# Kernel tuning notes

Measured on AMD Instinct MI355X. Metric: run time of the kernel, lower is better.

Reference implementation:

```python
import jax, jax.numpy as jnp
import numpy as np

B, N, C, H, K = 4, 16384, 256, 8, 64
D = C // H
EPS = 1e-8

def setup_inputs() -> dict:
    key = jax.random.key(0)
    ks = jax.random.split(key, 6)
    scale = 0.02
    return {
        "voxel_features": jax.random.normal(ks[0], (B, N, C), dtype=jnp.float32),
        "cluster_assignments": jax.random.uniform(ks[1], (B, N, K), dtype=jnp.float32),
        "w_qkv": jax.random.normal(ks[2], (C, 3 * C), dtype=jnp.float32) * scale,
        "w_proj": jax.random.normal(ks[3], (C, C), dtype=jnp.float32) * scale,
        "b_proj": jnp.zeros((C,), dtype=jnp.float32),
        "cluster_bias": jax.random.normal(ks[4], (K, K), dtype=jnp.float32) * scale,
    }

def reference(voxel_features, cluster_assignments, w_qkv, w_proj, b_proj, cluster_bias):
    b, n, c = voxel_features.shape
    h, d = H, c // H
    A = cluster_assignments                                  # (B,N,K)
    qkv = (voxel_features @ w_qkv).reshape(b, n, 3, h, d)    # (B,N,3,H,D)
    q = jnp.moveaxis(qkv[:, :, 0], 1, 2)                     # (B,H,N,D)
    k = jnp.moveaxis(qkv[:, :, 1], 1, 2)
    v = jnp.moveaxis(qkv[:, :, 2], 1, 2)
    # cluster mass per (batch, cluster)
    denom = A.sum(axis=1) + EPS                              # (B,K)
    # cluster-pooled K/V: contraction over N (the huge broadcast-sum in torch)
    k_cluster = jnp.einsum('bnk,bhnd->bhkd', A, k) / denom[:, None, :, None]
    v_cluster = jnp.einsum('bnk,bhnd->bhkd', A, v) / denom[:, None, :, None]
    attn = jnp.einsum('bhnd,bhkd->bhnk', q, k_cluster) * (d ** -0.5)
    bias = jnp.einsum('bnk,kl->bnl', A, cluster_bias)        # (B,N,K)
    attn = jax.nn.softmax(attn + bias[:, None, :, :], axis=-1)
    x = jnp.einsum('bhnk,bhkd->bhnd', attn, v_cluster)       # (B,H,N,D)
    x = jnp.moveaxis(x, 1, 2).reshape(b, n, c)               # (B,N,C)
    return x @ w_proj + b_proj
```

## Files before the change

### kernel.cpp

```cpp
#include <hip/hip_runtime.h>

#define NTOK 16384
#define BATCH 4

typedef __attribute__((ext_vector_type(8))) short bf16x8;
typedef __attribute__((ext_vector_type(8))) unsigned short ushort8;
typedef __attribute__((ext_vector_type(4))) float f32x4;

__device__ __forceinline__ unsigned short f2bf(float f) {
  union { float f; unsigned int u; } c; c.f = f;
  unsigned int r = c.u + 0x7fff + ((c.u >> 16) & 1);
  return (unsigned short)(r >> 16);
}

__global__ __launch_bounds__(256) void zero_f(float* __restrict__ p, int n) {
  int i = blockIdx.x * 256 + threadIdx.x;
  if (i < n) p[i] = 0.f;
}

__global__ __launch_bounds__(256) void convx(const float* __restrict__ in,
                                             unsigned short* __restrict__ out,
                                             int n8) {
  for (int i = blockIdx.x * 256 + threadIdx.x; i < n8; i += gridDim.x * 256) {
    float4 a = *(const float4*)(in + 8 * (size_t)i);
    float4 b = *(const float4*)(in + 8 * (size_t)i + 4);
    ushort8 o;
    o[0] = f2bf(a.x); o[1] = f2bf(a.y); o[2] = f2bf(a.z); o[3] = f2bf(a.w);
    o[4] = f2bf(b.x); o[5] = f2bf(b.y); o[6] = f2bf(b.z); o[7] = f2bf(b.w);
    *(ushort8*)(out + 8 * (size_t)i) = o;
  }
}

__global__ __launch_bounds__(256) void convw(const float* __restrict__ w_qkv,
                                             const float* __restrict__ w_proj,
                                             const float* __restrict__ cb,
                                             unsigned short* __restrict__ wqT,
                                             unsigned short* __restrict__ wpT,
                                             unsigned short* __restrict__ cbbT) {
  int n = blockIdx.x, k = threadIdx.x;
  if (n < 768) wqT[n * 256 + k] = f2bf(w_qkv[(size_t)k * 768 + n]);
  else if (n < 1024) wpT[(n - 768) * 256 + k] = f2bf(w_proj[(size_t)k * 256 + (n - 768)]);
  else if (k < 64) {
    for (int j = 0; j < 64; ++j) cbbT[k * 64 + j] = f2bf(cb[j * 64 + k]);
  }
}

template <int ADD_BIAS, int C_BF16>
__global__ __launch_bounds__(256, 2) void gemm_mfma(const unsigned short* __restrict__ Ab,
                                                    const unsigned short* __restrict__ BT,
                                                    const float* __restrict__ bias,
                                                    void* __restrict__ Cv,
                                                    int N, int K, int lda) {
  __shared__ unsigned short As[2][128][72];
  __shared__ unsigned short Bs[2][128][72];
  const int tid = threadIdx.x;
  int flat = blockIdx.y * gridDim.x + blockIdx.x;
  int xc = flat & 7, t = flat >> 3;
  int gx = gridDim.x, ypx = gridDim.y >> 3;
  int bx = t % gx, by = xc * ypx + t / gx;
  const int bn = bx * 128, bm = by * 128;
  const int lane = tid & 63;
  const int wv = tid >> 6;
  const int wm = wv & 1, wn = wv >> 1;
  const int m16 = lane & 15, quad = lane >> 4;

  const int srow = tid >> 1;
  const int scol = (tid & 1) * 32;

  ushort8 ra[4][4], rb[4][4];
  {
    const unsigned short* ga = Ab + (size_t)(bm + srow) * lda + scol;
    const unsigned short* gb = BT + (size_t)(bn + srow) * K + scol;
#pragma unroll
    for (int kt = 0; kt < 4; ++kt)
#pragma unroll
      for (int i = 0; i < 4; ++i) {
        ra[kt][i] = *(const ushort8*)(ga + kt * 64 + 8 * i);
        rb[kt][i] = *(const ushort8*)(gb + kt * 64 + 8 * i);
      }
  }

  f32x4 acc[4][4];
#pragma unroll
  for (int r = 0; r < 4; ++r)
#pragma unroll
    for (int c = 0; c < 4; ++c) acc[r][c] = (f32x4){0.f, 0.f, 0.f, 0.f};

#pragma unroll
  for (int kt = 0; kt < 4; ++kt) {
    const int bufi = kt & 1;
#pragma unroll
    for (int i = 0; i < 4; ++i) {
      *(ushort8*)&As[bufi][srow][scol + 8 * i] = ra[kt][i];
      *(ushort8*)&Bs[bufi][srow][scol + 8 * i] = rb[kt][i];
    }
    __syncthreads();
#pragma unroll
    for (int ks = 0; ks < 64; ks += 32) {
      bf16x8 af[4], bf[4];
#pragma unroll
      for (int r = 0; r < 4; ++r)
        af[r] = *(const bf16x8*)&As[bufi][wm * 64 + r * 16 + m16][ks + quad * 8];
#pragma unroll
      for (int c = 0; c < 4; ++c)
        bf[c] = *(const bf16x8*)&Bs[bufi][wn * 64 + c * 16 + m16][ks + quad * 8];
#pragma unroll
      for (int r = 0; r < 4; ++r)
#pragma unroll
        for (int c = 0; c < 4; ++c)
          acc[r][c] = __builtin_amdgcn_mfma_f32_16x16x32_bf16(af[r], bf[c], acc[r][c], 0, 0, 0);
    }
  }

#pragma unroll
  for (int c = 0; c < 4; ++c) {
    int col = bn + wn * 64 + c * 16 + m16;
    float bv = ADD_BIAS ? bias[col] : 0.f;
#pragma unroll
    for (int r = 0; r < 4; ++r) {
      int row0 = bm + wm * 64 + r * 16 + quad * 4;
#pragma unroll
      for (int i = 0; i < 4; ++i) {
        if (C_BF16)
          ((unsigned short*)Cv)[(size_t)(row0 + i) * N + col] = f2bf(acc[r][c][i] + bv);
        else
          ((float*)Cv)[(size_t)(row0 + i) * N + col] = acc[r][c][i] + bv;
      }
    }
  }
}

__global__ __launch_bounds__(256) void pool_mfma(const float* __restrict__ A,
                                                 const unsigned short* __restrict__ qkv,
                                                 float* __restrict__ part) {
  __shared__ unsigned short At[64][40];
  __shared__ unsigned short KVt[128][40];
  const int tid = threadIdx.x;
  const int tch = blockIdx.x, cblk = blockIdx.y, b = blockIdx.z;
  const int w = tid >> 6, lane = tid & 63;
  const int m16 = lane & 15, quad = lane >> 4;
  const size_t row0 = (size_t)b * NTOK + (size_t)tch * 256;
  const int cb0 = cblk * 128;

  f32x4 acc[4][2];
#pragma unroll
  for (int r = 0; r < 4; ++r)
#pragma unroll
    for (int c = 0; c < 2; ++c) acc[r][c] = (f32x4){0.f, 0.f, 0.f, 0.f};

  ushort8 pkv[2];
  float4 pav[2];
  auto loadG = [&](int t0) {
#pragma unroll
    for (int u = 0; u < 2; ++u) {
      int idx = tid + u * 256;
      int tok = idx & 31, g = idx >> 5;
      pkv[u] = *(const ushort8*)(qkv + (row0 + t0 + tok) * 768 + 256 + cb0 + g * 8);
      pav[u] = *(const float4*)(A + (row0 + t0 + tok) * 64 + g * 4);
    }
  };
  loadG(0);

  for (int ks = 0; ks < 8; ++ks) {
    __syncthreads();
#pragma unroll
    for (int u = 0; u < 2; ++u) {
      int idx = tid + u * 256;
      int tok = idx & 31, g = idx >> 5;
#pragma unroll
      for (int i = 0; i < 8; ++i) KVt[g * 8 + i][tok] = (unsigned short)pkv[u][i];
      At[g * 4 + 0][tok] = f2bf(pav[u].x);
      At[g * 4 + 1][tok] = f2bf(pav[u].y);
      At[g * 4 + 2][tok] = f2bf(pav[u].z);
      At[g * 4 + 3][tok] = f2bf(pav[u].w);
    }
    __syncthreads();
    if (ks + 1 < 8) loadG((ks + 1) * 32);
    bf16x8 af[4], bfr[2];
#pragma unroll
    for (int r = 0; r < 4; ++r) af[r] = *(const bf16x8*)&At[r * 16 + m16][quad * 8];
#pragma unroll
    for (int c = 0; c < 2; ++c) bfr[c] = *(const bf16x8*)&KVt[w * 32 + c * 16 + m16][quad * 8];
#pragma unroll
    for (int r = 0; r < 4; ++r)
#pragma unroll
      for (int c = 0; c < 2; ++c)
        acc[r][c] = __builtin_amdgcn_mfma_f32_16x16x32_bf16(af[r], bfr[c], acc[r][c], 0, 0, 0);
  }

  float* pp = part + (((size_t)b * 64 + tch) * 64) * 512 + cb0;
#pragma unroll
  for (int r = 0; r < 4; ++r)
#pragma unroll
    for (int c = 0; c < 2; ++c)
#pragma unroll
      for (int i = 0; i < 4; ++i) {
        int cl = r * 16 + quad * 4 + i;
        int ch = w * 32 + c * 16 + m16;
        pp[(size_t)cl * 512 + ch] = acc[r][c][i];
      }
}

__global__ __launch_bounds__(256) void pool2(const float* __restrict__ part,
                                             const float* __restrict__ asum,
                                             unsigned short* __restrict__ kcb,
                                             unsigned short* __restrict__ vcbT) {
  int id = blockIdx.x * 256 + threadIdx.x;
  int c = id & 511;
  int cl = (id >> 9) & 63;
  int b = id >> 15;
  const float* pp = part + ((size_t)b * 64 * 64 + cl) * 512 + c;
  float s = 0.f;
#pragma unroll 4
  for (int t = 0; t < 64; ++t) s += pp[(size_t)t * 32768];
  float denom = asum[b * 64 + cl] + 1e-8f;
  int p = c >> 8, h = (c >> 5) & 7, d = c & 31;
  if (p == 0)
    kcb[(((size_t)b * 8 + h) * 64 + cl) * 32 + d] = f2bf(s * 0.17677669529663687f / denom);
  else
    vcbT[(((size_t)b * 8 + h) * 32 + d) * 64 + cl] = f2bf(s / denom);
}

__global__ __launch_bounds__(256) void asum_kernel(const float* __restrict__ A,
                                                   float* __restrict__ asum) {
  __shared__ float red[4][64];
  const int ch = blockIdx.x, b = blockIdx.y;
  const int jq = threadIdx.x >> 6, k = threadIdx.x & 63;
  const size_t row0 = (size_t)b * NTOK + (size_t)ch * 256;
  const float* ap = A + (row0 + jq) * 64 + k;
  float s = 0.f;
#pragma unroll 4
  for (int j = 0; j < 64; ++j) s += ap[(size_t)j * 256];
  red[jq][k] = s;
  __syncthreads();
  if (threadIdx.x < 64) {
    float v = red[0][k] + red[1][k] + red[2][k] + red[3][k];
    atomicAdd(&asum[b * 64 + k], v);
  }
}

__global__ __launch_bounds__(256) void attn_mfma(const float* __restrict__ A,
                                                 unsigned short* __restrict__ qkv,
                                                 const unsigned short* __restrict__ kcb,
                                                 const unsigned short* __restrict__ vcbT,
                                                 const unsigned short* __restrict__ cbbT) {
  __shared__ __align__(16) char lds[62976];
  unsigned short* QA = (unsigned short*)lds;
  unsigned short* SB = (unsigned short*)(lds + 26624);
  float* S = (float*)lds;
  unsigned short* P = (unsigned short*)(lds + 39936);
  unsigned short* VT = (unsigned short*)(lds + 58368);

  const int tid = threadIdx.x;
  const int nb = blockIdx.x, h = blockIdx.y, b = blockIdx.z;
  const int w = tid >> 6, lane = tid & 63;
  const int m16 = lane & 15, quad = lane >> 4;
  const size_t row0 = (size_t)b * NTOK + (size_t)nb * 128;

  {
    int r = tid >> 1, half = tid & 1;
    const unsigned short* qp = qkv + (row0 + r) * 768 + h * 32 + half * 16;
    ushort8 q0 = *(const ushort8*)qp;
    ushort8 q1 = *(const ushort8*)(qp + 8);
    *(ushort8*)&QA[r * 104 + half * 16] = q0;
    *(ushort8*)&QA[r * 104 + half * 16 + 8] = q1;

    const float* ap = A + (row0 + r) * 64 + half * 32;
    unsigned short hb[32];
#pragma unroll
    for (int u = 0; u < 8; ++u) {
      float4 v = *(const float4*)(ap + 4 * u);
      hb[4 * u + 0] = f2bf(v.x); hb[4 * u + 1] = f2bf(v.y);
      hb[4 * u + 2] = f2bf(v.z); hb[4 * u + 3] = f2bf(v.w);
    }
#pragma unroll
    for (int u = 0; u < 4; ++u)
      *(ushort8*)&QA[r * 104 + 32 + half * 32 + 8 * u] = *(ushort8*)&hb[8 * u];

    if (tid < 64) {
      const unsigned short* kp = kcb + (((size_t)b * 8 + h) * 64 + tid) * 32;
#pragma unroll
      for (int u = 0; u < 4; ++u)
        *(ushort8*)&SB[tid * 104 + 8 * u] = *(const ushort8*)(kp + 8 * u);
    }
    if (tid < 128) {
      int l = tid >> 1, off = (tid & 1) * 32;
      const unsigned short* cp = cbbT + l * 64 + off;
#pragma unroll
      for (int u = 0; u < 4; ++u)
        *(ushort8*)&SB[l * 104 + 32 + off + 8 * u] = *(const ushort8*)(cp + 8 * u);
    }
    if (tid < 64) {
      int d = tid >> 1, off = (tid & 1) * 32;
      const unsigned short* vp = vcbT + (((size_t)b * 8 + h) * 32 + d) * 64 + off;
#pragma unroll
      for (int u = 0; u < 4; ++u)
        *(ushort8*)&VT[d * 72 + off + 8 * u] = *(const ushort8*)(vp + 8 * u);
    }
  }
  __syncthreads();

  f32x4 acc[2][4];
#pragma unroll
  for (int r = 0; r < 2; ++r)
#pragma unroll
    for (int c = 0; c < 4; ++c) acc[r][c] = (f32x4){0.f, 0.f, 0.f, 0.f};
#pragma unroll
  for (int kc3 = 0; kc3 < 96; kc3 += 32) {
    bf16x8 af[2], bf[4];
#pragma unroll
    for (int rt = 0; rt < 2; ++rt)
      af[rt] = *(const bf16x8*)&QA[(w * 32 + rt * 16 + m16) * 104 + kc3 + quad * 8];
#pragma unroll
    for (int nt = 0; nt < 4; ++nt)
      bf[nt] = *(const bf16x8*)&SB[(nt * 16 + m16) * 104 + kc3 + quad * 8];
#pragma unroll
    for (int rt = 0; rt < 2; ++rt)
#pragma unroll
      for (int nt = 0; nt < 4; ++nt)
        acc[rt][nt] = __builtin_amdgcn_mfma_f32_16x16x32_bf16(af[rt], bf[nt], acc[rt][nt], 0, 0, 0);
  }
  __syncthreads();

#pragma unroll
  for (int rt = 0; rt < 2; ++rt)
#pragma unroll
    for (int nt = 0; nt < 4; ++nt)
#pragma unroll
      for (int i = 0; i < 4; ++i)
        S[(w * 32 + rt * 16 + quad * 4 + i) * 68 + nt * 16 + m16] = acc[rt][nt][i];
  __syncthreads();

  if (tid < 128) {
    float sc[64];
#pragma unroll
    for (int u = 0; u < 16; ++u) *(float4*)(sc + 4 * u) = *(const float4*)&S[tid * 68 + 4 * u];
    float m = sc[0];
#pragma unroll
    for (int k = 1; k < 64; ++k) m = fmaxf(m, sc[k]);
    float l = 0.f;
#pragma unroll
    for (int k = 0; k < 64; ++k) {
      float e = __expf(sc[k] - m);
      sc[k] = e;
      l += e;
    }
    float rl = 1.f / l;
    unsigned short hp[64];
#pragma unroll
    for (int k = 0; k < 64; ++k) hp[k] = f2bf(sc[k] * rl);
#pragma unroll
    for (int u = 0; u < 8; ++u) *(ushort8*)&P[tid * 72 + 8 * u] = *(ushort8*)&hp[8 * u];
  }
  __syncthreads();

  f32x4 acc2[2][2];
#pragma unroll
  for (int r = 0; r < 2; ++r)
#pragma unroll
    for (int c = 0; c < 2; ++c) acc2[r][c] = (f32x4){0.f, 0.f, 0.f, 0.f};
#pragma unroll
  for (int kch = 0; kch < 64; kch += 32) {
    bf16x8 af2[2], bf2[2];
#pragma unroll
    for (int rt = 0; rt < 2; ++rt)
      af2[rt] = *(const bf16x8*)&P[(w * 32 + rt * 16 + m16) * 72 + kch + quad * 8];
#pragma unroll
    for (int nt = 0; nt < 2; ++nt)
      bf2[nt] = *(const bf16x8*)&VT[(nt * 16 + m16) * 72 + kch + quad * 8];
#pragma unroll
    for (int rt = 0; rt < 2; ++rt)
#pragma unroll
      for (int nt = 0; nt < 2; ++nt)
        acc2[rt][nt] = __builtin_amdgcn_mfma_f32_16x16x32_bf16(af2[rt], bf2[nt], acc2[rt][nt], 0, 0, 0);
  }

#pragma unroll
  for (int rt = 0; rt < 2; ++rt)
#pragma unroll
    for (int nt = 0; nt < 2; ++nt)
#pragma unroll
      for (int i = 0; i < 4; ++i) {
        int tr = w * 32 + rt * 16 + quad * 4 + i;
        int d = nt * 16 + m16;
        qkv[(row0 + tr) * 768 + h * 32 + d] = f2bf(acc2[rt][nt][i]);
      }
}

extern "C" void kernel_launch(void* const* d_in, const int* in_sizes, int n_in,
                              void* d_out, int out_size, void* d_ws, size_t ws_size,
                              hipStream_t stream) {
  const float* voxel  = (const float*)d_in[0];
  const float* A      = (const float*)d_in[1];
  const float* w_qkv  = (const float*)d_in[2];
  const float* w_proj = (const float*)d_in[3];
  const float* b_proj = (const float*)d_in[4];
  const float* cb     = (const float*)d_in[5];
  float* out = (float*)d_out;
  (void)in_sizes; (void)n_in; (void)out_size; (void)ws_size;

  char* wsb = (char*)d_ws;
  unsigned short* qkv = (unsigned short*)wsb;
  float* part = (float*)(wsb + 100663296);
  float* asum = (float*)(wsb + 100663296 + 33554432);
  unsigned short* wqT  = (unsigned short*)(wsb + 134218752);
  unsigned short* wpT  = wqT + 196608;
  unsigned short* kcb  = wpT + 65536;
  unsigned short* vcbT = kcb + 65536;
  unsigned short* cbbT = vcbT + 65536;
  unsigned short* xb = (unsigned short*)part;

  zero_f<<<1, 256, 0, stream>>>(asum, 256);
  convw<<<1025, 256, 0, stream>>>(w_qkv, w_proj, cb, wqT, wpT, cbbT);
  convx<<<2048, 256, 0, stream>>>(voxel, xb, 2097152);

  gemm_mfma<0, 1><<<dim3(6, 512), 256, 0, stream>>>(xb, wqT, nullptr, qkv,
                                                    768, 256, 256);

  asum_kernel<<<dim3(64, BATCH), 256, 0, stream>>>(A, asum);
  pool_mfma<<<dim3(64, 4, BATCH), 256, 0, stream>>>(A, qkv, part);
  pool2<<<512, 256, 0, stream>>>(part, asum, kcb, vcbT);

  attn_mfma<<<dim3(NTOK / 128, 8, BATCH), 256, 0, stream>>>(A, qkv, kcb, vcbT, cbbT);

  gemm_mfma<1, 0><<<dim3(2, 512), 256, 0, stream>>>(qkv, wpT, b_proj, out,
                                                    256, 256, 768);
}
```

Baseline: 289.9 us.

## Process four heads per attention block, reuse bias term, register-resident softmax

Result: faster. 270.1 us (-6.8%).

```diff
diff --git a/kernel.cpp b/kernel.cpp
--- a/kernel.cpp
+++ b/kernel.cpp
@@ -18,16 +18,20 @@
   if (i < n) p[i] = 0.f;
 }
 
-__global__ __launch_bounds__(256) void convx(const float* __restrict__ in,
-                                             unsigned short* __restrict__ out,
-                                             int n8) {
-  for (int i = blockIdx.x * 256 + threadIdx.x; i < n8; i += gridDim.x * 256) {
-    float4 a = *(const float4*)(in + 8 * (size_t)i);
-    float4 b = *(const float4*)(in + 8 * (size_t)i + 4);
+__global__ __launch_bounds__(256) void convx2(const float* __restrict__ voxel,
+                                              const float* __restrict__ A,
+                                              unsigned short* __restrict__ xb,
+                                              unsigned short* __restrict__ Ab) {
+  for (int i = blockIdx.x * 256 + threadIdx.x; i < 2621440; i += gridDim.x * 256) {
+    const float* src; unsigned short* dst; int j;
+    if (i < 2097152) { j = i; src = voxel; dst = xb; }
+    else { j = i - 2097152; src = A; dst = Ab; }
+    float4 a = *(const float4*)(src + 8 * (size_t)j);
+    float4 b = *(const float4*)(src + 8 * (size_t)j + 4);
     ushort8 o;
     o[0] = f2bf(a.x); o[1] = f2bf(a.y); o[2] = f2bf(a.z); o[3] = f2bf(a.w);
     o[4] = f2bf(b.x); o[5] = f2bf(b.y); o[6] = f2bf(b.z); o[7] = f2bf(b.w);
-    *(ushort8*)(out + 8 * (size_t)i) = o;
+    *(ushort8*)(dst + 8 * (size_t)j) = o;
   }
 }
 
@@ -239,152 +243,180 @@
   }
 }
 
-__global__ __launch_bounds__(256) void attn_mfma(const float* __restrict__ A,
+__global__ __launch_bounds__(256) void attn_mfma(const unsigned short* __restrict__ Ab,
                                                  unsigned short* __restrict__ qkv,
                                                  const unsigned short* __restrict__ kcb,
                                                  const unsigned short* __restrict__ vcbT,
                                                  const unsigned short* __restrict__ cbbT) {
-  __shared__ __align__(16) char lds[62976];
-  unsigned short* QA = (unsigned short*)lds;
-  unsigned short* SB = (unsigned short*)(lds + 26624);
-  float* S = (float*)lds;
-  unsigned short* P = (unsigned short*)(lds + 39936);
-  unsigned short* VT = (unsigned short*)(lds + 58368);
+  __shared__ __align__(16) char lds[38400];
+  unsigned short* PA  = (unsigned short*)lds;
+  unsigned short* Qs  = (unsigned short*)(lds + 18432);
+  unsigned short* KCs = (unsigned short*)(lds + 28672);
+  unsigned short* VTs = (unsigned short*)(lds + 33792);
+  unsigned short* CBs = (unsigned short*)(lds + 28672);
 
   const int tid = threadIdx.x;
-  const int nb = blockIdx.x, h = blockIdx.y, b = blockIdx.z;
+  const int nb = blockIdx.x, hq = blockIdx.y, b = blockIdx.z;
+  const int h0 = hq * 4;
   const int w = tid >> 6, lane = tid & 63;
   const int m16 = lane & 15, quad = lane >> 4;
   const size_t row0 = (size_t)b * NTOK + (size_t)nb * 128;
 
+  const int r2 = tid >> 1, half = tid & 1;
+  const int l4 = tid >> 2, s3 = tid & 3;
+  const int d8 = tid >> 3, s7 = tid & 7;
+
+  ushort8 rA[4], rcb[2];
   {
-    int r = tid >> 1, half = tid & 1;
-    const unsigned short* qp = qkv + (row0 + r) * 768 + h * 32 + half * 16;
-    ushort8 q0 = *(const ushort8*)qp;
-    ushort8 q1 = *(const ushort8*)(qp + 8);
-    *(ushort8*)&QA[r * 104 + half * 16] = q0;
-    *(ushort8*)&QA[r * 104 + half * 16 + 8] = q1;
-
-    const float* ap = A + (row0 + r) * 64 + half * 32;
-    unsigned short hb[32];
-#pragma unroll
-    for (int u = 0; u < 8; ++u) {
-      float4 v = *(const float4*)(ap + 4 * u);
-      hb[4 * u + 0] = f2bf(v.x); hb[4 * u + 1] = f2bf(v.y);
-      hb[4 * u + 2] = f2bf(v.z); hb[4 * u + 3] = f2bf(v.w);
-    }
-#pragma unroll
-    for (int u = 0; u < 4; ++u)
-      *(ushort8*)&QA[r * 104 + 32 + half * 32 + 8 * u] = *(ushort8*)&hb[8 * u];
-
-    if (tid < 64) {
-      const unsigned short* kp = kcb + (((size_t)b * 8 + h) * 64 + tid) * 32;
-#pragma unroll
-      for (int u = 0; u < 4; ++u)
-        *(ushort8*)&SB[tid * 104 + 8 * u] = *(const ushort8*)(kp + 8 * u);
-    }
-    if (tid < 128) {
-      int l = tid >> 1, off = (tid & 1) * 32;
-      const unsigned short* cp = cbbT + l * 64 + off;
-#pragma unroll
-      for (int u = 0; u < 4; ++u)
-        *(ushort8*)&SB[l * 104 + 32 + off + 8 * u] = *(const ushort8*)(cp + 8 * u);
-    }
-    if (tid < 64) {
-      int d = tid >> 1, off = (tid & 1) * 32;
-      const unsigned short* vp = vcbT + (((size_t)b * 8 + h) * 32 + d) * 64 + off;
-#pragma unroll
-      for (int u = 0; u < 4; ++u)
-        *(ushort8*)&VT[d * 72 + off + 8 * u] = *(const ushort8*)(vp + 8 * u);
-    }
-  }
+    const unsigned short* ap = Ab + (row0 + r2) * 64 + half * 32;
+#pragma unroll
+    for (int u = 0; u < 4; ++u) rA[u] = *(const ushort8*)(ap + 8 * u);
+    const unsigned short* cp = cbbT + l4 * 64 + s3 * 16;
+    rcb[0] = *(const ushort8*)cp;
+    rcb[1] = *(const ushort8*)(cp + 8);
+  }
+  ushort8 rq[2][2], rkc[2], rvt[2];
+  {
+    const unsigned short* qp = qkv + (row0 + r2) * 768 + h0 * 32 + half * 16;
+    rq[0][0] = *(const ushort8*)qp;
+    rq[0][1] = *(const ushort8*)(qp + 8);
+    rkc[0] = *(const ushort8*)(kcb + (((size_t)b * 8 + h0) * 64 + l4) * 32 + s3 * 8);
+    rvt[0] = *(const ushort8*)(vcbT + (((size_t)b * 8 + h0) * 32 + d8) * 64 + s7 * 8);
+  }
+#pragma unroll
+  for (int u = 0; u < 4; ++u) *(ushort8*)&PA[r2 * 72 + half * 32 + 8 * u] = rA[u];
+  *(ushort8*)&CBs[l4 * 72 + s3 * 16] = rcb[0];
+  *(ushort8*)&CBs[l4 * 72 + s3 * 16 + 8] = rcb[1];
   __syncthreads();
 
-  f32x4 acc[2][4];
-#pragma unroll
-  for (int r = 0; r < 2; ++r)
-#pragma unroll
-    for (int c = 0; c < 4; ++c) acc[r][c] = (f32x4){0.f, 0.f, 0.f, 0.f};
-#pragma unroll
-  for (int kc3 = 0; kc3 < 96; kc3 += 32) {
+  f32x4 bacc[2][4];
+#pragma unroll
+  for (int rt = 0; rt < 2; ++rt)
+#pragma unroll
+    for (int nt = 0; nt < 4; ++nt) bacc[rt][nt] = (f32x4){0.f, 0.f, 0.f, 0.f};
+#pragma unroll
+  for (int ks = 0; ks < 64; ks += 32) {
     bf16x8 af[2], bf[4];
 #pragma unroll
     for (int rt = 0; rt < 2; ++rt)
-      af[rt] = *(const bf16x8*)&QA[(w * 32 + rt * 16 + m16) * 104 + kc3 + quad * 8];
+      af[rt] = *(const bf16x8*)&PA[(w * 32 + rt * 16 + m16) * 72 + ks + quad * 8];
 #pragma unroll
     for (int nt = 0; nt < 4; ++nt)
-      bf[nt] = *(const bf16x8*)&SB[(nt * 16 + m16) * 104 + kc3 + quad * 8];
+      bf[nt] = *(const bf16x8*)&CBs[(nt * 16 + m16) * 72 + ks + quad * 8];
 #pragma unroll
     for (int rt = 0; rt < 2; ++rt)
 #pragma unroll
       for (int nt = 0; nt < 4; ++nt)
-        acc[rt][nt] = __builtin_amdgcn_mfma_f32_16x16x32_bf16(af[rt], bf[nt], acc[rt][nt], 0, 0, 0);
+        bacc[rt][nt] = __builtin_amdgcn_mfma_f32_16x16x32_bf16(af[rt], bf[nt], bacc[rt][nt], 0, 0, 0);
   }
   __syncthreads();
 
 #pragma unroll
-  for (int rt = 0; rt < 2; ++rt)
-#pragma unroll
-    for (int nt = 0; nt < 4; ++nt)
+  for (int hh = 0; hh < 4; ++hh) {
+    const int h = h0 + hh;
+    const int cur = hh & 1;
+    *(ushort8*)&Qs[r2 * 40 + half * 16] = rq[cur][0];
+    *(ushort8*)&Qs[r2 * 40 + half * 16 + 8] = rq[cur][1];
+    *(ushort8*)&KCs[l4 * 40 + s3 * 8] = rkc[cur];
+    *(ushort8*)&VTs[d8 * 72 + s7 * 8] = rvt[cur];
+    if (hh < 3) {
+      const int h1 = h + 1;
+      const unsigned short* qp = qkv + (row0 + r2) * 768 + h1 * 32 + half * 16;
+      rq[cur ^ 1][0] = *(const ushort8*)qp;
+      rq[cur ^ 1][1] = *(const ushort8*)(qp + 8);
+      rkc[cur ^ 1] = *(const ushort8*)(kcb + (((size_t)b * 8 + h1) * 64 + l4) * 32 + s3 * 8);
+      rvt[cur ^ 1] = *(const ushort8*)(vcbT + (((size_t)b * 8 + h1) * 32 + d8) * 64 + s7 * 8);
+    }
+    __syncthreads();
+
+    f32x4 acc[2][4];
+#pragma unroll
+    for (int rt = 0; rt < 2; ++rt)
+#pragma unroll
+      for (int nt = 0; nt < 4; ++nt) acc[rt][nt] = bacc[rt][nt];
+    {
+      bf16x8 af[2], bf[4];
+#pragma unroll
+      for (int rt = 0; rt < 2; ++rt)
+        af[rt] = *(const bf16x8*)&Qs[(w * 32 + rt * 16 + m16) * 40 + quad * 8];
+#pragma unroll
+      for (int nt = 0; nt < 4; ++nt)
+        bf[nt] = *(const bf16x8*)&KCs[(nt * 16 + m16) * 40 + quad * 8];
+#pragma unroll
+      for (int rt = 0; rt < 2; ++rt)
+#pragma unroll
+        for (int nt = 0; nt < 4; ++nt)
+          acc[rt][nt] = __builtin_amdgcn_mfma_f32_16x16x32_bf16(af[rt], bf[nt], acc[rt][nt], 0, 0, 0);
+    }
+
+#pragma unroll
+    for (int rt = 0; rt < 2; ++rt) {
+      f32x4 mxv, sv;
 #pragma unroll
       for (int i = 0; i < 4; ++i)
-        S[(w * 32 + rt * 16 + quad * 4 + i) * 68 + nt * 16 + m16] = acc[rt][nt][i];
-  __syncthreads();
-
-  if (tid < 128) {
-    float sc[64];
-#pragma unroll
-    for (int u = 0; u < 16; ++u) *(float4*)(sc + 4 * u) = *(const float4*)&S[tid * 68 + 4 * u];
-    float m = sc[0];
-#pragma unroll
-    for (int k = 1; k < 64; ++k) m = fmaxf(m, sc[k]);
-    float l = 0.f;
-#pragma unroll
-    for (int k = 0; k < 64; ++k) {
-      float e = __expf(sc[k] - m);
-      sc[k] = e;
-      l += e;
-    }
-    float rl = 1.f / l;
-    unsigned short hp[64];
-#pragma unroll
-    for (int k = 0; k < 64; ++k) hp[k] = f2bf(sc[k] * rl);
-#pragma unroll
-    for (int u = 0; u < 8; ++u) *(ushort8*)&P[tid * 72 + 8 * u] = *(ushort8*)&hp[8 * u];
-  }
-  __syncthreads();
-
-  f32x4 acc2[2][2];
-#pragma unroll
-  for (int r = 0; r < 2; ++r)
-#pragma unroll
-    for (int c = 0; c < 2; ++c) acc2[r][c] = (f32x4){0.f, 0.f, 0.f, 0.f};
-#pragma unroll
-  for (int kch = 0; kch < 64; kch += 32) {
-    bf16x8 af2[2], bf2[2];
+        mxv[i] = fmaxf(fmaxf(acc[rt][0][i], acc[rt][1][i]),
+                       fmaxf(acc[rt][2][i], acc[rt][3][i]));
+#pragma unroll
+      for (int msk = 1; msk < 16; msk <<= 1)
+#pragma unroll
+        for (int i = 0; i < 4; ++i) mxv[i] = fmaxf(mxv[i], __shfl_xor(mxv[i], msk));
+#pragma unroll
+      for (int i = 0; i < 4; ++i) sv[i] = 0.f;
+#pragma unroll
+      for (int nt = 0; nt < 4; ++nt)
+#pragma unroll
+        for (int i = 0; i < 4; ++i) {
+          float e = __expf(acc[rt][nt][i] - mxv[i]);
+          acc[rt][nt][i] = e;
+          sv[i] += e;
+        }
+#pragma unroll
+      for (int msk = 1; msk < 16; msk <<= 1)
+#pragma unroll
+        for (int i = 0; i < 4; ++i) sv[i] += __shfl_xor(sv[i], msk);
+#pragma unroll
+      for (int i = 0; i < 4; ++i) sv[i] = 1.f / sv[i];
+#pragma unroll
+      for (int nt = 0; nt < 4; ++nt)
+#pragma unroll
+        for (int i = 0; i < 4; ++i)
+          PA[(w * 32 + rt * 16 + quad * 4 + i) * 72 + nt * 16 + m16] =
+              f2bf(acc[rt][nt][i] * sv[i]);
+    }
+
+    f32x4 acc2[2][2];
 #pragma unroll
     for (int rt = 0; rt < 2; ++rt)
-      af2[rt] = *(const bf16x8*)&P[(w * 32 + rt * 16 + m16) * 72 + kch + quad * 8];
-#pragma unroll
-    for (int nt = 0; nt < 2; ++nt)
-      bf2[nt] = *(const bf16x8*)&VT[(nt * 16 + m16) * 72 + kch + quad * 8];
+#pragma unroll
+      for (int nt = 0; nt < 2; ++nt) acc2[rt][nt] = (f32x4){0.f, 0.f, 0.f, 0.f};
+#pragma unroll
+    for (int kch = 0; kch < 64; kch += 32) {
+      bf16x8 af2[2], bf2[2];
+#pragma unroll
+      for (int rt = 0; rt < 2; ++rt)
+        af2[rt] = *(const bf16x8*)&PA[(w * 32 + rt * 16 + m16) * 72 + kch + quad * 8];
+#pragma unroll
+      for (int nt = 0; nt < 2; ++nt)
+        bf2[nt] = *(const bf16x8*)&VTs[(nt * 16 + m16) * 72 + kch + quad * 8];
+#pragma unroll
+      for (int rt = 0; rt < 2; ++rt)
+#pragma unroll
+        for (int nt = 0; nt < 2; ++nt)
+          acc2[rt][nt] = __builtin_amdgcn_mfma_f32_16x16x32_bf16(af2[rt], bf2[nt], acc2[rt][nt], 0, 0, 0);
+    }
+
 #pragma unroll
     for (int rt = 0; rt < 2; ++rt)
 #pragma unroll
       for (int nt = 0; nt < 2; ++nt)
-        acc2[rt][nt] = __builtin_amdgcn_mfma_f32_16x16x32_bf16(af2[rt], bf2[nt], acc2[rt][nt], 0, 0, 0);
-  }
-
-#pragma unroll
-  for (int rt = 0; rt < 2; ++rt)
-#pragma unroll
-    for (int nt = 0; nt < 2; ++nt)
-#pragma unroll
-      for (int i = 0; i < 4; ++i) {
-        int tr = w * 32 + rt * 16 + quad * 4 + i;
-        int d = nt * 16 + m16;
-        qkv[(row0 + tr) * 768 + h * 32 + d] = f2bf(acc2[rt][nt][i]);
-      }
+#pragma unroll
+        for (int i = 0; i < 4; ++i) {
+          int tr = w * 32 + rt * 16 + quad * 4 + i;
+          int d = nt * 16 + m16;
+          qkv[(row0 + tr) * 768 + h * 32 + d] = f2bf(acc2[rt][nt][i]);
+        }
+    __syncthreads();
+  }
 }
 
 extern "C" void kernel_launch(void* const* d_in, const int* in_sizes, int n_in,
@@ -409,10 +441,11 @@
   unsigned short* vcbT = kcb + 65536;
   unsigned short* cbbT = vcbT + 65536;
   unsigned short* xb = (unsigned short*)part;
+  unsigned short* Ab = (unsigned short*)d_out;
 
   zero_f<<<1, 256, 0, stream>>>(asum, 256);
   convw<<<1025, 256, 0, stream>>>(w_qkv, w_proj, cb, wqT, wpT, cbbT);
-  convx<<<2048, 256, 0, stream>>>(voxel, xb, 2097152);
+  convx2<<<2048, 256, 0, stream>>>(voxel, A, xb, Ab);
 
   gemm_mfma<0, 1><<<dim3(6, 512), 256, 0, stream>>>(xb, wqT, nullptr, qkv,
                                                     768, 256, 256);
@@ -421,7 +454,7 @@
   pool_mfma<<<dim3(64, 4, BATCH), 256, 0, stream>>>(A, qkv, part);
   pool2<<<512, 256, 0, stream>>>(part, asum, kcb, vcbT);
 
-  attn_mfma<<<dim3(NTOK / 128, 8, BATCH), 256, 0, stream>>>(A, qkv, kcb, vcbT, cbbT);
+  attn_mfma<<<dim3(NTOK / 128, 2, BATCH), 256, 0, stream>>>(Ab, qkv, kcb, vcbT, cbbT);
 
   gemm_mfma<1, 0><<<dim3(2, 512), 256, 0, stream>>>(qkv, wpT, b_proj, out,
                                                     256, 256, 768);
```
